# Optimization experiments

Measured on AMD Instinct MI355X. Metric: run time of the kernel, lower is better.

Reference implementation:

```python
import jax, jax.numpy as jnp
import numpy as np
from jax import lax

T_D = 0.7          # condensation radius
T_B = 0.2          # min beta to seed a condensate
FEATURE_LENGTH = 9 # columns of raw features before the prediction block
N_FEAT = 17        # n_ccoords = N_FEAT - 14 = 3
N_EVENTS = 16
POINTS_PER_EVENT = 65536


def setup_inputs() -> dict:
    key = jax.random.key(0)
    N = N_EVENTS * POINTS_PER_EVENT
    # uniform [0,1): betas in [0,1), ccoords in the unit cube -> realistic clustering
    x = jax.random.uniform(key, (N, N_FEAT), dtype=jnp.float32)
    row_splits = (jnp.arange(N_EVENTS + 1) * POINTS_PER_EVENT).astype(jnp.int32)
    return {"x": x, "row_splits": row_splits}


def _build_condensates(ccoords, betas, radius, min_beta):
    """Greedy NMS-like condensation, vectorized over events.
    ccoords: [E, P, C] float; betas: [E, P] float.
    Returns asso [E,P] int32 (index of assigned condensate, -1 = noise) and
    iscond [E,P] bool (condensation point flags).
    """
    E, P, _ = ccoords.shape
    r2 = radius * radius

    def masked_beta(asso):
        return jnp.where(asso < 0, betas, -1.0)

    def cond_fn(state):
        asso, _ = state
        return jnp.any(jnp.max(masked_beta(asso), axis=1) >= min_beta)

    def body_fn(state):
        asso, iscond = state
        mb = masked_beta(asso)                     # [E,P]
        ref = jnp.argmax(mb, axis=1)               # [E] highest-beta unassigned point
        valid = jnp.take_along_axis(mb, ref[:, None], axis=1)[:, 0] >= min_beta  # [E]
        refc = jnp.take_along_axis(ccoords, ref[:, None, None], axis=1)          # [E,1,C]
        distsq = jnp.sum((ccoords - refc) ** 2, axis=-1)                          # [E,P]
        assign = (asso < 0) & (distsq <= r2) & valid[:, None]
        asso = jnp.where(assign, ref[:, None].astype(jnp.int32), asso)
        newcond = (jnp.arange(P)[None, :] == ref[:, None]) & valid[:, None]
        return asso, iscond | newcond

    asso0 = jnp.full((E, P), -1, dtype=jnp.int32)
    iscond0 = jnp.zeros((E, P), dtype=jnp.bool_)
    return lax.while_loop(cond_fn, body_fn, (asso0, iscond0))


def reference(x, row_splits):
    E = row_splits.shape[0] - 1
    N, F = x.shape
    P = N // E  # uniform events (RaggedConstructTensor equivalent for equal splits)
    n_ccoords = F - 14
    x_pred = x[:, FEATURE_LENGTH:]
    n_pred = x_pred.shape[-1]
    betas = x_pred[:, 0].reshape(E, P)
    ccoords = x_pred[:, n_pred - n_ccoords:].reshape(E, P, n_ccoords)

    asso, iscond = _build_condensates(ccoords, betas, T_D, T_B)

    ncond = jnp.sum(iscond, axis=1).astype(jnp.int32)  # condensates per event
    out_row_splits = jnp.concatenate(
        [jnp.zeros((1,), jnp.int32), jnp.cumsum(ncond).astype(jnp.int32)])
    # jit-safe equivalent of dout = x[iscond > 0]: zero-mask non-condensates
    mask = iscond.reshape(-1, 1).astype(x.dtype)
    dout = x * mask  # [N, F], rows of non-condensates are zero
    return dout, out_row_splits
```

## Files before the change

kernel.cpp:

```cpp
#include <hip/hip_runtime.h>

typedef unsigned long long u64;
typedef unsigned int u32;

static constexpr int NF = 17;
static constexpr int BCOL = 9;
static constexpr int CCOL = 14;
static constexpr int CONDCAP = 256;
static constexpr int NPASS = 2;
static constexpr int RPB = 512;
static constexpr int MAXIT = 8;
static constexpr int CHK = 8;

#define T_B_F ((float)0.2)
#define R2_F  ((float)(0.7*0.7))

__device__ __forceinline__ u64 kmax(u64 a, u64 b){ return a > b ? a : b; }

__device__ __forceinline__ u64 shfl_down_u64(u64 v, int off){
    u32 lo = (u32)v, hi = (u32)(v >> 32);
    lo = __shfl_down(lo, off, 64);
    hi = __shfl_down(hi, off, 64);
    return ((u64)hi << 32) | lo;
}

__device__ __forceinline__ u64 waveReduceMax(u64 k){
    #pragma unroll
    for (int off = 32; off > 0; off >>= 1){
        u64 o = shfl_down_u64(k, off);
        if (o > k) k = o;
    }
    return k;
}

__device__ __forceinline__ float dist2(float cx, float cy, float cz,
                                       float rx, float ry, float rz){
    #pragma clang fp contract(off)
    float dx = cx - rx, dy = cy - ry, dz = cz - rz;
    float sx = dx * dx, sy = dy * dy, sz = dz * dz;
    return (sx + sy) + sz;
}

__device__ __forceinline__ u64 makeKey(float beta, u32 idx){
    return ((u64)__float_as_uint(beta) << 32) | (u64)(0xFFFFFFFFu - idx);
}

__global__ void k_init(u32* ws){
    int t = threadIdx.x;
    if (t < 1024) ws[t] = 0;
}

__global__ __launch_bounds__(256) void k_filter(
    const float4* __restrict__ x4, float4* __restrict__ out4,
    u64* __restrict__ argmax0, int* __restrict__ cnt0,
    float4* __restrict__ cA, int* __restrict__ iA,
    int P, int chunksPerEvent)
{
    __shared__ float4 lrow[RPB];
    __shared__ int swc[4], swb[4], sbase;
    __shared__ u64 sred[4];

    int e = blockIdx.x / chunksPerEvent;
    int chunk = blockIdx.x % chunksPerEvent;
    int rowStart = chunk * RPB;
    size_t tile4 = (size_t)blockIdx.x * (RPB * NF / 4);

    const int N4 = RPB * NF / 4;
    float4 z = make_float4(0.f, 0.f, 0.f, 0.f);
    for (int i = threadIdx.x; i < N4; i += 256){
        float4 v = x4[tile4 + i];
        out4[tile4 + i] = z;
        float vv[4] = {v.x, v.y, v.z, v.w};
        int f0 = 4 * i;
        #pragma unroll
        for (int j = 0; j < 4; j++){
            int flat = f0 + j;
            int row = flat / NF;
            int col = flat - row * NF;
            if (col == BCOL)       ((float*)&lrow[row])[3] = vv[j];
            else if (col >= CCOL)  ((float*)&lrow[row])[col - CCOL] = vv[j];
        }
    }
    __syncthreads();

    int tid = threadIdx.x, lid = tid & 63, wid = tid >> 6;
    float4 a0 = lrow[tid], a1 = lrow[tid + 256];
    bool k0 = (a0.w >= T_B_F), k1 = (a1.w >= T_B_F);
    u64 bal0 = __ballot(k0), bal1 = __ballot(k1);
    int wcnt = __popcll(bal0) + __popcll(bal1);

    u64 lk = 0;
    if (k0) lk = makeKey(a0.w, (u32)(rowStart + tid));
    if (k1) lk = kmax(lk, makeKey(a1.w, (u32)(rowStart + tid + 256)));
    u64 kw = waveReduceMax(lk);
    if (lid == 0){ swc[wid] = wcnt; sred[wid] = kw; }
    __syncthreads();
    if (tid == 0){
        int tot = 0;
        for (int w = 0; w < 4; w++){ swb[w] = tot; tot += swc[w]; }
        sbase = tot ? atomicAdd(&cnt0[e], tot) : 0;
        u64 m = sred[0];
        for (int i = 1; i < 4; i++) m = kmax(m, sred[i]);
        if (m) atomicMax(&argmax0[e], m);
    }
    __syncthreads();
    int base = sbase + swb[wid];
    u64 lm = (1ull << lid) - 1;
    size_t eoff = (size_t)e * P;
    if (k0){
        int pos = base + __popcll(bal0 & lm);
        cA[eoff + pos] = a0;
        iA[eoff + pos] = rowStart + tid;
    }
    if (k1){
        int pos = base + __popcll(bal0) + __popcll(bal1 & lm);
        cA[eoff + pos] = a1;
        iA[eoff + pos] = rowStart + tid + 256;
    }
}

__global__ __launch_bounds__(256) void k_pass(
    const float* __restrict__ x,
    const float4* __restrict__ cIn, const int* __restrict__ iIn,
    float4* __restrict__ cOut, int* __restrict__ iOut,
    const u64* __restrict__ argmaxIn, u64* __restrict__ argmaxOut,
    const int* __restrict__ cntIn, int* __restrict__ cntOut,
    int* __restrict__ ncond, int* __restrict__ condlist,
    int P, int blocksPerEvent)
{
    __shared__ int swc[4], swb[4], sbase;
    __shared__ u64 sred[4];

    int e = blockIdx.x / blocksPerEvent;
    int c = blockIdx.x % blocksPerEvent;
    u64 key = argmaxIn[e];
    float betaRef = __uint_as_float((u32)(key >> 32));
    if (!(betaRef >= T_B_F)) return;
    u32 refIdx = 0xFFFFFFFFu - (u32)(key & 0xFFFFFFFFu);
    if (c == 0 && threadIdx.x == 0){
        int s = atomicAdd(&ncond[e], 1);
        if (s < CONDCAP) condlist[e * CONDCAP + s] = (int)refIdx;
    }
    size_t rbase = ((size_t)e * P + refIdx) * NF;
    float rx = x[rbase + CCOL], ry = x[rbase + CCOL + 1], rz = x[rbase + CCOL + 2];

    int n = cntIn[e];
    int tid = threadIdx.x, lid = tid & 63, wid = tid >> 6;
    size_t eoff = (size_t)e * P;
    int stride = blocksPerEvent * 256;

    float4 cc[MAXIT]; int ix[MAXIT]; bool kp[MAXIT]; u64 bal[MAXIT];
    int wcnt = 0;
    u64 lk = 0;
    #pragma unroll
    for (int k = 0; k < MAXIT; k++){
        int i = c * 256 + tid + k * stride;
        bool inb = i < n;
        int ii = inb ? i : 0;
        cc[k] = cIn[eoff + ii];
        ix[k] = iIn[eoff + ii];
        float d2 = dist2(cc[k].x, cc[k].y, cc[k].z, rx, ry, rz);
        kp[k] = inb && !(d2 <= R2_F);
        bal[k] = __ballot(kp[k]);
        wcnt += __popcll(bal[k]);
        if (kp[k]) lk = kmax(lk, makeKey(cc[k].w, (u32)ix[k]));
    }
    u64 kw = waveReduceMax(lk);
    if (lid == 0){ swc[wid] = wcnt; sred[wid] = kw; }
    __syncthreads();
    if (tid == 0){
        int tot = 0;
        for (int w = 0; w < 4; w++){ swb[w] = tot; tot += swc[w]; }
        sbase = tot ? atomicAdd(&cntOut[e], tot) : 0;
        u64 m = sred[0];
        for (int i = 1; i < 4; i++) m = kmax(m, sred[i]);
        if (m) atomicMax(&argmaxOut[e], m);
    }
    __syncthreads();
    int pos = sbase + swb[wid];
    u64 lm = (1ull << lid) - 1;
    #pragma unroll
    for (int k = 0; k < MAXIT; k++){
        if (kp[k]){
            int p_ = pos + __popcll(bal[k] & lm);
            cOut[eoff + p_] = cc[k];
            iOut[eoff + p_] = ix[k];
        }
        pos += __popcll(bal[k]);
    }
}

__global__ __launch_bounds__(1024) void k_finish(
    const float* __restrict__ x, float* __restrict__ out,
    float4* cA, int* iA, float4* cB, int* iB,
    const u64* __restrict__ argmaxN, const int* __restrict__ cntN,
    int* __restrict__ ncond, int* __restrict__ condlist,
    int* __restrict__ done, int P, int E)
{
    int e = blockIdx.x;
    __shared__ u64 skey16[16];
    __shared__ float4 spay16[16];
    __shared__ int scnt, sNC, sLast;
    __shared__ u64 skey;
    __shared__ float srefc[3];

    int tid = threadIdx.x, lid = tid & 63, wid = tid >> 6;
    int n = cntN[e];
    u64 key = argmaxN[e];
    float4* cIn = cA + (size_t)e * P; int* iIn = iA + (size_t)e * P;
    float4* cOut = cB + (size_t)e * P; int* iOut = iB + (size_t)e * P;
    bool havePay = false;

    while (true){
        float betaRef = __uint_as_float((u32)(key >> 32));
        if (!(betaRef >= T_B_F)) break;
        u32 refIdx = 0xFFFFFFFFu - (u32)(key & 0xFFFFFFFFu);
        if (tid == 0){
            int s = atomicAdd(&ncond[e], 1);
            if (s < CONDCAP) condlist[e * CONDCAP + s] = (int)refIdx;
            if (!havePay){
                size_t rb = ((size_t)e * P + refIdx) * NF;
                srefc[0] = x[rb + CCOL];
                srefc[1] = x[rb + CCOL + 1];
                srefc[2] = x[rb + CCOL + 2];
            }
            scnt = 0;
        }
        havePay = true;
        __syncthreads();
        float rx = srefc[0], ry = srefc[1], rz = srefc[2];

        u64 bk = 0; float bx = 0.f, by = 0.f, bz = 0.f;
        for (int base = 0; base < n; base += 1024 * CHK){
            float4 cc[CHK]; int ix[CHK]; bool kp[CHK]; u64 bal[CHK];
            int wcnt = 0;
            #pragma unroll
            for (int k = 0; k < CHK; k++){
                int i = base + k * 1024 + tid;
                bool inb = i < n;
                int ii = inb ? i : 0;
                cc[k] = cIn[ii];
                ix[k] = iIn[ii];
                float d2 = dist2(cc[k].x, cc[k].y, cc[k].z, rx, ry, rz);
                kp[k] = inb && !(d2 <= R2_F);
                bal[k] = __ballot(kp[k]);
                wcnt += __popcll(bal[k]);
                if (kp[k]){
                    u64 mk = makeKey(cc[k].w, (u32)ix[k]);
                    if (mk > bk){ bk = mk; bx = cc[k].x; by = cc[k].y; bz = cc[k].z; }
                }
            }
            int wbase = 0;
            if (lid == 0) wbase = wcnt ? atomicAdd(&scnt, wcnt) : 0;
            wbase = __shfl(wbase, 0, 64);
            u64 lm = (1ull << lid) - 1;
            #pragma unroll
            for (int k = 0; k < CHK; k++){
                if (kp[k]){
                    int p_ = wbase + __popcll(bal[k] & lm);
                    cOut[p_] = cc[k];
                    iOut[p_] = ix[k];
                }
                wbase += __popcll(bal[k]);
            }
        }
        #pragma unroll
        for (int off = 32; off > 0; off >>= 1){
            u64 ok = shfl_down_u64(bk, off);
            float ox = __shfl_down(bx, off, 64);
            float oy = __shfl_down(by, off, 64);
            float oz = __shfl_down(bz, off, 64);
            if (ok > bk){ bk = ok; bx = ox; by = oy; bz = oz; }
        }
        if (lid == 0){ skey16[wid] = bk; spay16[wid] = make_float4(bx, by, bz, 0.f); }
        __syncthreads();
        if (tid == 0){
            u64 m = 0; float4 pp = make_float4(0.f, 0.f, 0.f, 0.f);
            for (int i = 0; i < 16; i++)
                if (skey16[i] > m){ m = skey16[i]; pp = spay16[i]; }
            skey = m;
            srefc[0] = pp.x; srefc[1] = pp.y; srefc[2] = pp.z;
        }
        __syncthreads();
        key = skey;
        n = scnt;
        { float4* t = cIn; cIn = cOut; cOut = t; }
        { int* t = iIn; iIn = iOut; iOut = t; }
        __syncthreads();
    }

    if (tid == 0) sNC = atomicAdd(&ncond[e], 0);
    __syncthreads();
    int nc = sNC; if (nc > CONDCAP) nc = CONDCAP;
    for (int i = tid; i < nc * NF; i += 1024){
        int j = i / NF, f = i - j * NF;
        int row = condlist[e * CONDCAP + j];
        size_t b = ((size_t)e * P + row) * NF;
        out[b + f] = x[b + f];
    }

    __threadfence();
    if (tid == 0) sLast = atomicAdd(done, 1);
    __syncthreads();
    if (sLast == E - 1 && tid == 0){
        size_t so = (size_t)E * P * NF;
        int s = 0;
        out[so] = 0.f;
        for (int i = 0; i < E; i++){
            s += atomicAdd(&ncond[i], 0);
            out[so + i + 1] = (float)s;
        }
    }
}

extern "C" void kernel_launch(void* const* d_in, const int* in_sizes, int n_in,
                              void* d_out, int out_size, void* d_ws, size_t ws_size,
                              hipStream_t stream) {
    const float* x = (const float*)d_in[0];
    int N = in_sizes[0] / NF;
    int E = in_sizes[1] - 1;
    int P = N / E;
    float* out = (float*)d_out;
    char* ws = (char*)d_ws;

    u64* argmax = (u64*)ws;
    int* cnt    = (int*)(ws + 1024);
    int* ncond  = (int*)(ws + 2048);
    int* done   = (int*)(ws + 2560);
    int* condlist = (int*)(ws + 4096);
    size_t listOff = 32768;
    size_t listElems = (size_t)E * P;
    float4* cA = (float4*)(ws + listOff);
    float4* cB = (float4*)(ws + listOff + listElems * 16);
    int* iA = (int*)(ws + listOff + listElems * 32);
    int* iB = (int*)(ws + listOff + listElems * 36);

    k_init<<<1, 1024, 0, stream>>>((u32*)ws);

    int chunksPerEvent = P / RPB;
    k_filter<<<E * chunksPerEvent, 256, 0, stream>>>(
        (const float4*)x, (float4*)out, argmax, cnt, cA, iA, P, chunksPerEvent);

    int bpe = 32;
    float4* cs[2] = {cA, cB};
    int* is[2] = {iA, iB};
    for (int r = 0; r < NPASS; r++){
        k_pass<<<E * bpe, 256, 0, stream>>>(
            x, cs[r & 1], is[r & 1], cs[(r + 1) & 1], is[(r + 1) & 1],
            argmax + r * E, argmax + (r + 1) * E,
            cnt + r * E, cnt + (r + 1) * E,
            ncond, condlist, P, bpe);
    }

    k_finish<<<E, 1024, 0, stream>>>(
        x, out, cA, iA, cB, iB, argmax + NPASS * E, cnt + NPASS * E,
        ncond, condlist, done, P, E);
}
```

Measured before the change: 207.1 us.

## Replace per-iteration global passes with beta-histogram top-chunk LDS NMS

Builds a per-event beta histogram in the filter kernel. It then picks the top ~4096 candidates and runs the greedy condensation entirely in shared memory. A parallel suppress kernel removes all remaining candidates covered by those references, and a second in-LDS NMS handles the survivors. Output zeroing moves to a separate non-temporal store kernel. This removes the serial global-memory scan per condensate, at the cost of more complex logic, a REFCAP/SCAP capacity limit, and a risk of ordering mismatches if the survivors exceed the caps.

```diff
diff --git a/kernel.cpp b/kernel.cpp
--- a/kernel.cpp
+++ b/kernel.cpp
@@ -2,35 +2,26 @@
 
 typedef unsigned long long u64;
 typedef unsigned int u32;
+typedef float f4n __attribute__((ext_vector_type(4)));
 
 static constexpr int NF = 17;
 static constexpr int BCOL = 9;
 static constexpr int CCOL = 14;
-static constexpr int CONDCAP = 256;
-static constexpr int NPASS = 2;
 static constexpr int RPB = 512;
-static constexpr int MAXIT = 8;
-static constexpr int CHK = 8;
+static constexpr int CHUNK = 4096;
+static constexpr int REFCAP = 64;
+static constexpr int SCAP = 32768;
+static constexpr int SUP_BPE = 32;
+static constexpr int SUP_CHK = 8;
 
 #define T_B_F ((float)0.2)
 #define R2_F  ((float)(0.7*0.7))
-
-__device__ __forceinline__ u64 kmax(u64 a, u64 b){ return a > b ? a : b; }
 
 __device__ __forceinline__ u64 shfl_down_u64(u64 v, int off){
     u32 lo = (u32)v, hi = (u32)(v >> 32);
     lo = __shfl_down(lo, off, 64);
     hi = __shfl_down(hi, off, 64);
     return ((u64)hi << 32) | lo;
-}
-
-__device__ __forceinline__ u64 waveReduceMax(u64 k){
-    #pragma unroll
-    for (int off = 32; off > 0; off >>= 1){
-        u64 o = shfl_down_u64(k, off);
-        if (o > k) k = o;
-    }
-    return k;
 }
 
 __device__ __forceinline__ float dist2(float cx, float cy, float cz,
@@ -45,31 +36,88 @@
     return ((u64)__float_as_uint(beta) << 32) | (u64)(0xFFFFFFFFu - idx);
 }
 
+__device__ __forceinline__ int bucketOf(float b){
+    int v = (int)((b - 0.2f) * 320.0f);
+    return v > 255 ? 255 : v;
+}
+
+__device__ int lds_nms(float* cbx, float* cby, float* cbz, float* cbb, int* cbi,
+                       int m, u64* rkey, int* rslot, u64* skey, int* sslot,
+                       float4* refs_xyz, int* refs_idx, int refbase, int nref)
+{
+    int tid = threadIdx.x, lid = tid & 63, wid = tid >> 6;
+    int nw = blockDim.x >> 6;
+    for (int round = 0; round < REFCAP; round++){
+        u64 bk = 0; int bs = -1;
+        for (int k = tid; k < m; k += blockDim.x){
+            float b = cbb[k];
+            if (b >= 0.f){
+                u64 kk = makeKey(b, (u32)cbi[k]);
+                if (kk > bk){ bk = kk; bs = k; }
+            }
+        }
+        #pragma unroll
+        for (int off = 32; off > 0; off >>= 1){
+            u64 ok = shfl_down_u64(bk, off);
+            int os = __shfl_down(bs, off, 64);
+            if (ok > bk){ bk = ok; bs = os; }
+        }
+        if (lid == 0){ rkey[wid] = bk; rslot[wid] = bs; }
+        __syncthreads();
+        if (tid == 0){
+            u64 mb = 0; int ms = -1;
+            for (int i = 0; i < nw; i++) if (rkey[i] > mb){ mb = rkey[i]; ms = rslot[i]; }
+            *skey = mb; *sslot = ms;
+        }
+        __syncthreads();
+        if (*skey == 0) break;
+        int rs = *sslot;
+        float rx = cbx[rs], ry = cby[rs], rz = cbz[rs];
+        if (tid == 0 && nref < REFCAP){
+            refs_xyz[refbase + nref] = make_float4(rx, ry, rz, 0.f);
+            refs_idx[refbase + nref] = cbi[rs];
+        }
+        nref++;
+        for (int k = tid; k < m; k += blockDim.x){
+            if (cbb[k] >= 0.f && dist2(cbx[k], cby[k], cbz[k], rx, ry, rz) <= R2_F)
+                cbb[k] = -1.f;
+        }
+        __syncthreads();
+    }
+    return nref;
+}
+
 __global__ void k_init(u32* ws){
-    int t = threadIdx.x;
-    if (t < 1024) ws[t] = 0;
+    for (int i = threadIdx.x; i < 4352; i += 1024) ws[i] = 0;
+}
+
+__global__ __launch_bounds__(256) void k_zero(f4n* __restrict__ out4, int n4){
+    int i = blockIdx.x * 256 + threadIdx.x;
+    int stride = gridDim.x * 256;
+    f4n z = {0.f, 0.f, 0.f, 0.f};
+    for (; i < n4; i += stride) __builtin_nontemporal_store(z, &out4[i]);
 }
 
 __global__ __launch_bounds__(256) void k_filter(
-    const float4* __restrict__ x4, float4* __restrict__ out4,
-    u64* __restrict__ argmax0, int* __restrict__ cnt0,
-    float4* __restrict__ cA, int* __restrict__ iA,
+    const float4* __restrict__ x4,
+    int* __restrict__ cnt, int* __restrict__ hist,
+    float4* __restrict__ cand_xyz, int* __restrict__ cand_idx,
     int P, int chunksPerEvent)
 {
     __shared__ float4 lrow[RPB];
+    __shared__ int lh[256];
     __shared__ int swc[4], swb[4], sbase;
-    __shared__ u64 sred[4];
 
     int e = blockIdx.x / chunksPerEvent;
     int chunk = blockIdx.x % chunksPerEvent;
     int rowStart = chunk * RPB;
     size_t tile4 = (size_t)blockIdx.x * (RPB * NF / 4);
+    int tid = threadIdx.x;
+    lh[tid] = 0;
 
     const int N4 = RPB * NF / 4;
-    float4 z = make_float4(0.f, 0.f, 0.f, 0.f);
-    for (int i = threadIdx.x; i < N4; i += 256){
+    for (int i = tid; i < N4; i += 256){
         float4 v = x4[tile4 + i];
-        out4[tile4 + i] = z;
         float vv[4] = {v.x, v.y, v.z, v.w};
         int f0 = 4 * i;
         #pragma unroll
@@ -83,25 +131,19 @@
     }
     __syncthreads();
 
-    int tid = threadIdx.x, lid = tid & 63, wid = tid >> 6;
+    int lid = tid & 63, wid = tid >> 6;
     float4 a0 = lrow[tid], a1 = lrow[tid + 256];
     bool k0 = (a0.w >= T_B_F), k1 = (a1.w >= T_B_F);
     u64 bal0 = __ballot(k0), bal1 = __ballot(k1);
     int wcnt = __popcll(bal0) + __popcll(bal1);
-
-    u64 lk = 0;
-    if (k0) lk = makeKey(a0.w, (u32)(rowStart + tid));
-    if (k1) lk = kmax(lk, makeKey(a1.w, (u32)(rowStart + tid + 256)));
-    u64 kw = waveReduceMax(lk);
-    if (lid == 0){ swc[wid] = wcnt; sred[wid] = kw; }
+    if (k0) atomicAdd(&lh[bucketOf(a0.w)], 1);
+    if (k1) atomicAdd(&lh[bucketOf(a1.w)], 1);
+    if (lid == 0) swc[wid] = wcnt;
     __syncthreads();
     if (tid == 0){
         int tot = 0;
         for (int w = 0; w < 4; w++){ swb[w] = tot; tot += swc[w]; }
-        sbase = tot ? atomicAdd(&cnt0[e], tot) : 0;
-        u64 m = sred[0];
-        for (int i = 1; i < 4; i++) m = kmax(m, sred[i]);
-        if (m) atomicMax(&argmax0[e], m);
+        sbase = tot ? atomicAdd(&cnt[e], tot) : 0;
     }
     __syncthreads();
     int base = sbase + swb[wid];
@@ -109,197 +151,224 @@
     size_t eoff = (size_t)e * P;
     if (k0){
         int pos = base + __popcll(bal0 & lm);
-        cA[eoff + pos] = a0;
-        iA[eoff + pos] = rowStart + tid;
+        cand_xyz[eoff + pos] = a0;
+        cand_idx[eoff + pos] = rowStart + tid;
     }
     if (k1){
         int pos = base + __popcll(bal0) + __popcll(bal1 & lm);
-        cA[eoff + pos] = a1;
-        iA[eoff + pos] = rowStart + tid + 256;
-    }
-}
-
-__global__ __launch_bounds__(256) void k_pass(
-    const float* __restrict__ x,
-    const float4* __restrict__ cIn, const int* __restrict__ iIn,
-    float4* __restrict__ cOut, int* __restrict__ iOut,
-    const u64* __restrict__ argmaxIn, u64* __restrict__ argmaxOut,
-    const int* __restrict__ cntIn, int* __restrict__ cntOut,
-    int* __restrict__ ncond, int* __restrict__ condlist,
-    int P, int blocksPerEvent)
+        cand_xyz[eoff + pos] = a1;
+        cand_idx[eoff + pos] = rowStart + tid + 256;
+    }
+    if (lh[tid]) atomicAdd(&hist[e * 256 + tid], lh[tid]);
+}
+
+__global__ __launch_bounds__(1024) void k_nms1(
+    const int* __restrict__ hist, const float4* __restrict__ cand_xyz,
+    const int* __restrict__ cand_idx, const int* __restrict__ cnt,
+    float4* __restrict__ refs_xyz, int* __restrict__ refs_idx,
+    int* __restrict__ nref1, int* __restrict__ cutoffB, int P)
 {
+    __shared__ float cbx[CHUNK], cby[CHUNK], cbz[CHUNK], cbb[CHUNK];
+    __shared__ int cbi[CHUNK];
+    __shared__ int lh[256];
+    __shared__ int scut, sm;
+    __shared__ u64 rkey[16]; __shared__ int rslot[16];
+    __shared__ u64 skey; __shared__ int sslot;
+
+    int e = blockIdx.x, tid = threadIdx.x;
+    if (tid < 256) lh[tid] = hist[e * 256 + tid];
+    if (tid == 0) sm = 0;
+    __syncthreads();
+    if (tid == 0){
+        int tot = 0, c = 0;
+        for (int b = 255; b >= 0; b--){
+            if (tot + lh[b] > CHUNK){ c = b + 1; break; }
+            tot += lh[b];
+        }
+        scut = c;
+    }
+    __syncthreads();
+    int cut = scut, n = cnt[e];
+    size_t eoff = (size_t)e * P;
+    int lid = tid & 63;
+    for (int i0 = 0; i0 < n; i0 += 1024){
+        int i = i0 + tid;
+        bool sel = false; float4 v = make_float4(0.f, 0.f, 0.f, 0.f);
+        if (i < n){
+            v = cand_xyz[eoff + i];
+            sel = bucketOf(v.w) >= cut;
+        }
+        u64 bal = __ballot(sel);
+        int cw = __popcll(bal);
+        int base = 0;
+        if (lid == 0) base = cw ? atomicAdd(&sm, cw) : 0;
+        base = __shfl(base, 0, 64);
+        if (sel){
+            int pos = base + __popcll(bal & ((1ull << lid) - 1));
+            cbx[pos] = v.x; cby[pos] = v.y; cbz[pos] = v.z; cbb[pos] = v.w;
+            cbi[pos] = cand_idx[eoff + i];
+        }
+    }
+    __syncthreads();
+    int m = sm;
+    int nref = lds_nms(cbx, cby, cbz, cbb, cbi, m, rkey, rslot, &skey, &sslot,
+                       refs_xyz, refs_idx, e * REFCAP, 0);
+    if (tid == 0){ nref1[e] = nref; cutoffB[e] = cut; }
+}
+
+__global__ __launch_bounds__(256) void k_suppress(
+    const float4* __restrict__ cand_xyz, const int* __restrict__ cand_idx,
+    const int* __restrict__ cnt, const float4* __restrict__ refs_xyz,
+    const int* __restrict__ nref1, const int* __restrict__ cutoffB,
+    float4* __restrict__ surv_xyz, int* __restrict__ surv_idx,
+    int* __restrict__ survcnt, int P)
+{
+    __shared__ float4 lref[REFCAP];
     __shared__ int swc[4], swb[4], sbase;
-    __shared__ u64 sred[4];
-
-    int e = blockIdx.x / blocksPerEvent;
-    int c = blockIdx.x % blocksPerEvent;
-    u64 key = argmaxIn[e];
-    float betaRef = __uint_as_float((u32)(key >> 32));
-    if (!(betaRef >= T_B_F)) return;
-    u32 refIdx = 0xFFFFFFFFu - (u32)(key & 0xFFFFFFFFu);
-    if (c == 0 && threadIdx.x == 0){
-        int s = atomicAdd(&ncond[e], 1);
-        if (s < CONDCAP) condlist[e * CONDCAP + s] = (int)refIdx;
-    }
-    size_t rbase = ((size_t)e * P + refIdx) * NF;
-    float rx = x[rbase + CCOL], ry = x[rbase + CCOL + 1], rz = x[rbase + CCOL + 2];
-
-    int n = cntIn[e];
+    int e = blockIdx.x / SUP_BPE, c = blockIdx.x % SUP_BPE;
+    int nr = nref1[e], cut = cutoffB[e], n = cnt[e];
+    for (int i = threadIdx.x; i < nr; i += 256) lref[i] = refs_xyz[e * REFCAP + i];
+    __syncthreads();
     int tid = threadIdx.x, lid = tid & 63, wid = tid >> 6;
     size_t eoff = (size_t)e * P;
-    int stride = blocksPerEvent * 256;
-
-    float4 cc[MAXIT]; int ix[MAXIT]; bool kp[MAXIT]; u64 bal[MAXIT];
+    int stride = SUP_BPE * 256;
+
+    float4 cc[SUP_CHK]; int ix[SUP_CHK]; bool kp[SUP_CHK]; u64 bal[SUP_CHK];
     int wcnt = 0;
-    u64 lk = 0;
     #pragma unroll
-    for (int k = 0; k < MAXIT; k++){
+    for (int k = 0; k < SUP_CHK; k++){
         int i = c * 256 + tid + k * stride;
         bool inb = i < n;
         int ii = inb ? i : 0;
-        cc[k] = cIn[eoff + ii];
-        ix[k] = iIn[eoff + ii];
-        float d2 = dist2(cc[k].x, cc[k].y, cc[k].z, rx, ry, rz);
-        kp[k] = inb && !(d2 <= R2_F);
-        bal[k] = __ballot(kp[k]);
+        float4 v = cand_xyz[eoff + ii];
+        bool keep = inb && (bucketOf(v.w) < cut);
+        if (keep){
+            for (int r = 0; r < nr; r++){
+                float4 rf = lref[r];
+                if (dist2(v.x, v.y, v.z, rf.x, rf.y, rf.z) <= R2_F){ keep = false; break; }
+            }
+        }
+        cc[k] = v; kp[k] = keep;
+        bal[k] = __ballot(keep);
         wcnt += __popcll(bal[k]);
-        if (kp[k]) lk = kmax(lk, makeKey(cc[k].w, (u32)ix[k]));
-    }
-    u64 kw = waveReduceMax(lk);
-    if (lid == 0){ swc[wid] = wcnt; sred[wid] = kw; }
+        ix[k] = keep ? cand_idx[eoff + ii] : 0;
+    }
+    if (lid == 0) swc[wid] = wcnt;
     __syncthreads();
     if (tid == 0){
         int tot = 0;
         for (int w = 0; w < 4; w++){ swb[w] = tot; tot += swc[w]; }
-        sbase = tot ? atomicAdd(&cntOut[e], tot) : 0;
-        u64 m = sred[0];
-        for (int i = 1; i < 4; i++) m = kmax(m, sred[i]);
-        if (m) atomicMax(&argmaxOut[e], m);
+        sbase = tot ? atomicAdd(&survcnt[e], tot) : 0;
     }
     __syncthreads();
     int pos = sbase + swb[wid];
     u64 lm = (1ull << lid) - 1;
+    size_t soff = (size_t)e * SCAP;
     #pragma unroll
-    for (int k = 0; k < MAXIT; k++){
+    for (int k = 0; k < SUP_CHK; k++){
         if (kp[k]){
             int p_ = pos + __popcll(bal[k] & lm);
-            cOut[eoff + p_] = cc[k];
-            iOut[eoff + p_] = ix[k];
+            if (p_ < SCAP){ surv_xyz[soff + p_] = cc[k]; surv_idx[soff + p_] = ix[k]; }
         }
         pos += __popcll(bal[k]);
     }
 }
 
-__global__ __launch_bounds__(1024) void k_finish(
+__global__ __launch_bounds__(1024) void k_nms2(
     const float* __restrict__ x, float* __restrict__ out,
-    float4* cA, int* iA, float4* cB, int* iB,
-    const u64* __restrict__ argmaxN, const int* __restrict__ cntN,
-    int* __restrict__ ncond, int* __restrict__ condlist,
-    int* __restrict__ done, int P, int E)
+    const float4* __restrict__ surv_xyz, const int* __restrict__ surv_idx,
+    const int* __restrict__ survcnt,
+    float4* __restrict__ scr_xyz, int* __restrict__ scr_idx,
+    float4* __restrict__ refs_xyz, int* __restrict__ refs_idx,
+    const int* __restrict__ nref1,
+    int* __restrict__ ncond, int* __restrict__ done, int P, int E)
 {
-    int e = blockIdx.x;
-    __shared__ u64 skey16[16];
-    __shared__ float4 spay16[16];
-    __shared__ int scnt, sNC, sLast;
-    __shared__ u64 skey;
-    __shared__ float srefc[3];
-
-    int tid = threadIdx.x, lid = tid & 63, wid = tid >> 6;
-    int n = cntN[e];
-    u64 key = argmaxN[e];
-    float4* cIn = cA + (size_t)e * P; int* iIn = iA + (size_t)e * P;
-    float4* cOut = cB + (size_t)e * P; int* iOut = iB + (size_t)e * P;
-    bool havePay = false;
-
-    while (true){
-        float betaRef = __uint_as_float((u32)(key >> 32));
-        if (!(betaRef >= T_B_F)) break;
-        u32 refIdx = 0xFFFFFFFFu - (u32)(key & 0xFFFFFFFFu);
-        if (tid == 0){
-            int s = atomicAdd(&ncond[e], 1);
-            if (s < CONDCAP) condlist[e * CONDCAP + s] = (int)refIdx;
-            if (!havePay){
-                size_t rb = ((size_t)e * P + refIdx) * NF;
-                srefc[0] = x[rb + CCOL];
-                srefc[1] = x[rb + CCOL + 1];
-                srefc[2] = x[rb + CCOL + 2];
-            }
-            scnt = 0;
-        }
-        havePay = true;
-        __syncthreads();
-        float rx = srefc[0], ry = srefc[1], rz = srefc[2];
-
-        u64 bk = 0; float bx = 0.f, by = 0.f, bz = 0.f;
-        for (int base = 0; base < n; base += 1024 * CHK){
-            float4 cc[CHK]; int ix[CHK]; bool kp[CHK]; u64 bal[CHK];
-            int wcnt = 0;
-            #pragma unroll
-            for (int k = 0; k < CHK; k++){
-                int i = base + k * 1024 + tid;
-                bool inb = i < n;
-                int ii = inb ? i : 0;
-                cc[k] = cIn[ii];
-                ix[k] = iIn[ii];
-                float d2 = dist2(cc[k].x, cc[k].y, cc[k].z, rx, ry, rz);
-                kp[k] = inb && !(d2 <= R2_F);
-                bal[k] = __ballot(kp[k]);
-                wcnt += __popcll(bal[k]);
-                if (kp[k]){
-                    u64 mk = makeKey(cc[k].w, (u32)ix[k]);
-                    if (mk > bk){ bk = mk; bx = cc[k].x; by = cc[k].y; bz = cc[k].z; }
-                }
-            }
-            int wbase = 0;
-            if (lid == 0) wbase = wcnt ? atomicAdd(&scnt, wcnt) : 0;
-            wbase = __shfl(wbase, 0, 64);
-            u64 lm = (1ull << lid) - 1;
-            #pragma unroll
-            for (int k = 0; k < CHK; k++){
-                if (kp[k]){
-                    int p_ = wbase + __popcll(bal[k] & lm);
-                    cOut[p_] = cc[k];
-                    iOut[p_] = ix[k];
-                }
-                wbase += __popcll(bal[k]);
-            }
+    __shared__ float cbx[CHUNK], cby[CHUNK], cbz[CHUNK], cbb[CHUNK];
+    __shared__ int cbi[CHUNK];
+    __shared__ u64 rkey[16]; __shared__ int rslot[16];
+    __shared__ u64 skey; __shared__ int sslot;
+    __shared__ int scnt2, sLast;
+
+    int e = blockIdx.x, tid = threadIdx.x, lid = tid & 63, wid = tid >> 6;
+    int m = survcnt[e]; if (m > SCAP) m = SCAP;
+    size_t soff = (size_t)e * SCAP;
+    int nref = nref1[e];
+
+    const float4* sx = surv_xyz + soff;
+    const int* si = surv_idx + soff;
+    float4* fbx[2] = {scr_xyz + (size_t)e * P, scr_xyz + (size_t)e * P + SCAP};
+    int* fbi[2] = {scr_idx + (size_t)e * P, scr_idx + (size_t)e * P + SCAP};
+    int pp = 0;
+
+    while (m > CHUNK){
+        u64 bk = 0; int bs = -1;
+        for (int i = tid; i < m; i += 1024){
+            float4 v = sx[i];
+            u64 kk = makeKey(v.w, (u32)si[i]);
+            if (kk > bk){ bk = kk; bs = i; }
         }
         #pragma unroll
         for (int off = 32; off > 0; off >>= 1){
             u64 ok = shfl_down_u64(bk, off);
-            float ox = __shfl_down(bx, off, 64);
-            float oy = __shfl_down(by, off, 64);
-            float oz = __shfl_down(bz, off, 64);
-            if (ok > bk){ bk = ok; bx = ox; by = oy; bz = oz; }
-        }
-        if (lid == 0){ skey16[wid] = bk; spay16[wid] = make_float4(bx, by, bz, 0.f); }
+            int os = __shfl_down(bs, off, 64);
+            if (ok > bk){ bk = ok; bs = os; }
+        }
+        if (lid == 0){ rkey[wid] = bk; rslot[wid] = bs; }
         __syncthreads();
         if (tid == 0){
-            u64 m = 0; float4 pp = make_float4(0.f, 0.f, 0.f, 0.f);
-            for (int i = 0; i < 16; i++)
-                if (skey16[i] > m){ m = skey16[i]; pp = spay16[i]; }
-            skey = m;
-            srefc[0] = pp.x; srefc[1] = pp.y; srefc[2] = pp.z;
-        }
-        __syncthreads();
-        key = skey;
-        n = scnt;
-        { float4* t = cIn; cIn = cOut; cOut = t; }
-        { int* t = iIn; iIn = iOut; iOut = t; }
-        __syncthreads();
-    }
-
-    if (tid == 0) sNC = atomicAdd(&ncond[e], 0);
-    __syncthreads();
-    int nc = sNC; if (nc > CONDCAP) nc = CONDCAP;
-    for (int i = tid; i < nc * NF; i += 1024){
+            u64 mb = 0; int ms = -1;
+            for (int i = 0; i < 16; i++) if (rkey[i] > mb){ mb = rkey[i]; ms = rslot[i]; }
+            sslot = ms; scnt2 = 0;
+        }
+        __syncthreads();
+        float4 rv = sx[sslot];
+        if (tid == 0 && nref < REFCAP){
+            refs_xyz[e * REFCAP + nref] = make_float4(rv.x, rv.y, rv.z, 0.f);
+            refs_idx[e * REFCAP + nref] = si[sslot];
+        }
+        nref++;
+        __syncthreads();
+        for (int i0 = 0; i0 < m; i0 += 1024){
+            int i = i0 + tid;
+            bool keep = false; float4 v = make_float4(0.f,0.f,0.f,0.f); int id_ = 0;
+            if (i < m){
+                v = sx[i]; id_ = si[i];
+                keep = !(dist2(v.x, v.y, v.z, rv.x, rv.y, rv.z) <= R2_F);
+            }
+            u64 bal = __ballot(keep);
+            int cw = __popcll(bal);
+            int b_ = 0;
+            if (lid == 0) b_ = cw ? atomicAdd(&scnt2, cw) : 0;
+            b_ = __shfl(b_, 0, 64);
+            if (keep){
+                int p_ = b_ + __popcll(bal & ((1ull << lid) - 1));
+                fbx[pp][p_] = v; fbi[pp][p_] = id_;
+            }
+        }
+        __syncthreads();
+        m = scnt2;
+        sx = fbx[pp]; si = fbi[pp]; pp ^= 1;
+        __syncthreads();
+    }
+
+    for (int i = tid; i < m; i += 1024){
+        float4 v = sx[i];
+        cbx[i] = v.x; cby[i] = v.y; cbz[i] = v.z; cbb[i] = v.w;
+        cbi[i] = si[i];
+    }
+    __syncthreads();
+    nref = lds_nms(cbx, cby, cbz, cbb, cbi, m, rkey, rslot, &skey, &sslot,
+                   refs_xyz, refs_idx, e * REFCAP, nref);
+
+    for (int i = tid; i < nref * NF; i += 1024){
         int j = i / NF, f = i - j * NF;
-        int row = condlist[e * CONDCAP + j];
+        int row = refs_idx[e * REFCAP + j];
         size_t b = ((size_t)e * P + row) * NF;
         out[b + f] = x[b + f];
     }
-
+    if (tid == 0) atomicExch(&ncond[e], nref);
     __threadfence();
+    __syncthreads();
     if (tid == 0) sLast = atomicAdd(done, 1);
     __syncthreads();
     if (sLast == E - 1 && tid == 0){
@@ -323,36 +392,38 @@
     float* out = (float*)d_out;
     char* ws = (char*)d_ws;
 
-    u64* argmax = (u64*)ws;
-    int* cnt    = (int*)(ws + 1024);
-    int* ncond  = (int*)(ws + 2048);
-    int* done   = (int*)(ws + 2560);
-    int* condlist = (int*)(ws + 4096);
-    size_t listOff = 32768;
-    size_t listElems = (size_t)E * P;
-    float4* cA = (float4*)(ws + listOff);
-    float4* cB = (float4*)(ws + listOff + listElems * 16);
-    int* iA = (int*)(ws + listOff + listElems * 32);
-    int* iB = (int*)(ws + listOff + listElems * 36);
+    int* cnt     = (int*)(ws + 0);
+    int* survcnt = (int*)(ws + 64);
+    int* ncond   = (int*)(ws + 128);
+    int* done    = (int*)(ws + 192);
+    int* nref1   = (int*)(ws + 256);
+    int* cutoffB = (int*)(ws + 320);
+    int* hist    = (int*)(ws + 1024);
+    float4* refs_xyz = (float4*)(ws + 20480);
+    int* refs_idx    = (int*)(ws + 36864);
+    size_t o = 65536;
+    float4* cand_xyz = (float4*)(ws + o);
+    int* cand_idx    = (int*)(ws + o + (size_t)E*P*16);
+    float4* surv_xyz = (float4*)(ws + o + (size_t)E*P*20);
+    int* surv_idx    = (int*)(ws + o + (size_t)E*P*20 + (size_t)E*SCAP*16);
 
     k_init<<<1, 1024, 0, stream>>>((u32*)ws);
+
+    int n4 = (N * NF) / 4;
+    k_zero<<<2048, 256, 0, stream>>>((f4n*)out, n4);
 
     int chunksPerEvent = P / RPB;
     k_filter<<<E * chunksPerEvent, 256, 0, stream>>>(
-        (const float4*)x, (float4*)out, argmax, cnt, cA, iA, P, chunksPerEvent);
-
-    int bpe = 32;
-    float4* cs[2] = {cA, cB};
-    int* is[2] = {iA, iB};
-    for (int r = 0; r < NPASS; r++){
-        k_pass<<<E * bpe, 256, 0, stream>>>(
-            x, cs[r & 1], is[r & 1], cs[(r + 1) & 1], is[(r + 1) & 1],
-            argmax + r * E, argmax + (r + 1) * E,
-            cnt + r * E, cnt + (r + 1) * E,
-            ncond, condlist, P, bpe);
-    }
-
-    k_finish<<<E, 1024, 0, stream>>>(
-        x, out, cA, iA, cB, iB, argmax + NPASS * E, cnt + NPASS * E,
-        ncond, condlist, done, P, E);
-}
+        (const float4*)x, cnt, hist, cand_xyz, cand_idx, P, chunksPerEvent);
+
+    k_nms1<<<E, 1024, 0, stream>>>(
+        hist, cand_xyz, cand_idx, cnt, refs_xyz, refs_idx, nref1, cutoffB, P);
+
+    k_suppress<<<E * SUP_BPE, 256, 0, stream>>>(
+        cand_xyz, cand_idx, cnt, refs_xyz, nref1, cutoffB,
+        surv_xyz, surv_idx, survcnt, P);
+
+    k_nms2<<<E, 1024, 0, stream>>>(
+        x, out, surv_xyz, surv_idx, survcnt, cand_xyz, cand_idx,
+        refs_xyz, refs_idx, nref1, ncond, done, P, E);
+}
```

Result: slower. 244.5 us (+18.1%).
